# Kernel optimization log

Hardware: AMD Instinct MI355X
Metric: run time of the kernel (lower is better)

Reference implementation:

```python
import math
import jax, jax.numpy as jnp
import numpy as np

B, S, HID = 2, 2048, 1024
NH, HD = 16, 64            # num heads, head dim (HID = NH*HD)
NB, MAXD = 32, 128         # relative attention buckets / max distance
Q_SCALING = 1.0


def setup_inputs() -> dict:
    key = jax.random.key(0)
    ks = jax.random.split(key, 6)
    return {
        "hidden_states": jax.random.normal(ks[0], (B, S, HID), dtype=jnp.float32),
        "w_qkv": jax.random.normal(ks[1], (HID, 3 * HID), dtype=jnp.float32) * 0.02,
        "b_qkv": jax.random.normal(ks[2], (3 * HID,), dtype=jnp.float32) * 0.02,
        "w_dense": jax.random.normal(ks[3], (HID, HID), dtype=jnp.float32) * 0.02,
        "b_dense": jax.random.normal(ks[4], (HID,), dtype=jnp.float32) * 0.02,
        "rel_attn_table": jax.random.normal(ks[5], (NH, NB), dtype=jnp.float32) * 0.02,
    }


def _relative_position_bucket(q_len, k_len, num_buckets, max_distance):
    # Bidirectional T5-style buckets, matching compute_relative_bias.
    ctx = jnp.arange(q_len, dtype=jnp.int32)[:, None]
    mem = jnp.arange(k_len, dtype=jnp.int32)[None, :]
    rel = mem - ctx                                     # [Q, K]
    nb = num_buckets // 2
    buckets = jnp.where(rel > 0, nb, 0)
    rel = jnp.abs(rel)
    max_exact = nb // 2
    is_small = rel < max_exact
    # log path (clamp to >=1 to avoid log(0); masked by is_small anyway)
    tmp = jnp.log(jnp.maximum(rel, 1).astype(jnp.float32) / max_exact)
    large = tmp / math.log(max_distance / max_exact) * (nb - max_exact)
    large = max_exact + large.astype(jnp.int32)
    large = jnp.minimum(large, nb - 1)
    return buckets + jnp.where(is_small, rel, large)    # [Q, K]


def reference(hidden_states, w_qkv, b_qkv, w_dense, b_dense, rel_attn_table):
    b, s, _ = hidden_states.shape
    qkv = hidden_states @ w_qkv + b_qkv                 # [B, S, 3*HID]
    q, k, v = jnp.split(qkv, 3, axis=-1)
    q = q.reshape(b, s, NH, HD)
    k = k.reshape(b, s, NH, HD)
    v = v.reshape(b, s, NH, HD)

    norm = Q_SCALING * math.sqrt(HD)
    scores = jnp.einsum("bqhd,bkhd->bhqk", q, k) / norm  # [B, H, S, S]

    buckets = _relative_position_bucket(s, s, NB, MAXD)  # [Q, K] int32
    bias = rel_attn_table[:, buckets]                    # [H, Q, K]
    scores = scores + bias[None]

    probs = jax.nn.softmax(scores, axis=-1)
    ctx = jnp.einsum("bhqk,bkhd->bqhd", probs, v).reshape(b, s, HID)
    return ctx @ w_dense + b_dense
```

## Files before the change

### kernel.cpp

```cpp
#include <hip/hip_runtime.h>
#include <hip/hip_bf16.h>
#include <math.h>

#define S_ 2048

typedef __attribute__((ext_vector_type(8))) short bf16x8;
typedef __attribute__((ext_vector_type(4))) float f32x4;
typedef __attribute__((ext_vector_type(8))) unsigned short u16x8;
typedef __attribute__((ext_vector_type(4))) unsigned short u16x4;

__device__ inline unsigned short f2bf(float f) {
  union { float f; unsigned u; } x; x.f = f;
  unsigned r = x.u + 0x7fff + ((x.u >> 16) & 1);
  return (unsigned short)(r >> 16);
}

__device__ __forceinline__ void gll16(const unsigned short* g, unsigned short* l) {
  __builtin_amdgcn_global_load_lds(
      (const __attribute__((address_space(1))) unsigned int*)g,
      (__attribute__((address_space(3))) unsigned int*)l, 16, 0, 0);
}

__global__ void bias_table_kernel(const float* __restrict__ table,
                                  float* __restrict__ biasTab) {
  int idx = blockIdx.x * blockDim.x + threadIdx.x;
  if (idx >= 16 * 4096) return;
  int h = idx >> 12;
  int r = idx & 4095;
  int rel = r - 2047;
  int bucket = rel > 0 ? 16 : 0;
  int ar = rel < 0 ? -rel : rel;
  if (ar < 8) {
    bucket += ar;
  } else {
    float tmp = logf((float)ar / 8.0f);
    float lf = tmp / 2.7725887222397811f * 8.0f;
    int large = 8 + (int)lf;
    bucket += (large < 15 ? large : 15);
  }
  biasTab[idx] = table[h * 32 + bucket];
}

__global__ __launch_bounds__(256) void cvt_bf16_kernel(
    const float* __restrict__ in, unsigned short* __restrict__ out, int n8) {
  int i = blockIdx.x * blockDim.x + threadIdx.x;
  if (i >= n8) return;
  float4 a = ((const float4*)in)[i * 2];
  float4 b = ((const float4*)in)[i * 2 + 1];
  u16x8 o;
  o[0] = f2bf(a.x); o[1] = f2bf(a.y); o[2] = f2bf(a.z); o[3] = f2bf(a.w);
  o[4] = f2bf(b.x); o[5] = f2bf(b.y); o[6] = f2bf(b.z); o[7] = f2bf(b.w);
  *(u16x8*)&out[(size_t)i * 8] = o;
}

__global__ __launch_bounds__(256) void transpose_cvt_kernel(
    const float* __restrict__ in, unsigned short* __restrict__ out,
    int K, int N) {
  __shared__ unsigned short tile[64][72];
  const int k0 = blockIdx.y * 64, n0 = blockIdx.x * 64;
  const int tid = threadIdx.x;
  const int rr = tid >> 4, cc = (tid & 15) * 4;
#pragma unroll
  for (int p = 0; p < 4; ++p) {
    int k = rr + p * 16;
    float4 v = *(const float4*)&in[(size_t)(k0 + k) * N + n0 + cc];
    tile[k][cc + 0] = f2bf(v.x);
    tile[k][cc + 1] = f2bf(v.y);
    tile[k][cc + 2] = f2bf(v.z);
    tile[k][cc + 3] = f2bf(v.w);
  }
  __syncthreads();
#pragma unroll
  for (int p = 0; p < 4; ++p) {
    int n = rr + p * 16;
    u16x4 o;
    o[0] = tile[cc + 0][n];
    o[1] = tile[cc + 1][n];
    o[2] = tile[cc + 2][n];
    o[3] = tile[cc + 3][n];
    *(u16x4*)&out[(size_t)(n0 + n) * K + k0 + cc] = o;
  }
}

template <bool BF16OUT>
__global__ __launch_bounds__(256) void gemm_mfma_kernel(
    const unsigned short* __restrict__ A, const unsigned short* __restrict__ Bt,
    const float* __restrict__ bias, void* __restrict__ Cout,
    int M, int N, int K) {
  __shared__ __align__(16) unsigned short As[128 * 32];
  __shared__ __align__(16) unsigned short Bs[128 * 32];
  const int tid = threadIdx.x;
  const int wave = tid >> 6, lane = tid & 63;
  const int lg = lane >> 4, lr = lane & 15;
  const int m0 = blockIdx.y * 128, n0 = blockIdx.x * 128;
  const int wm = (wave & 1) * 64, wn = (wave >> 1) * 64;

  f32x4 acc[4][4] = {};

  const int r0 = tid >> 2;
  const int sw = ((tid & 3) ^ (r0 & 3)) << 3;
  const unsigned short* aP0 = A + (size_t)(m0 + r0) * K + sw;
  const unsigned short* aP1 = A + (size_t)(m0 + 64 + r0) * K + sw;
  const unsigned short* bP0 = Bt + (size_t)(n0 + r0) * K + sw;
  const unsigned short* bP1 = Bt + (size_t)(n0 + 64 + r0) * K + sw;
  unsigned short* ldsA0 = &As[(tid & ~63) * 8];
  unsigned short* ldsA1 = &As[(256 + (tid & ~63)) * 8];
  unsigned short* ldsB0 = &Bs[(tid & ~63) * 8];
  unsigned short* ldsB1 = &Bs[(256 + (tid & ~63)) * 8];

  const int swz = (lg ^ (lr & 3)) << 3;

  for (int kt = 0; kt < K; kt += 32) {
    __syncthreads();
    gll16(aP0 + kt, ldsA0);
    gll16(aP1 + kt, ldsA1);
    gll16(bP0 + kt, ldsB0);
    gll16(bP1 + kt, ldsB1);
    __syncthreads();
    bf16x8 af[4], bfr[4];
#pragma unroll
    for (int t = 0; t < 4; ++t) {
      af[t]  = *(const bf16x8*)&As[(wm + t * 16 + lr) * 32 + swz];
      bfr[t] = *(const bf16x8*)&Bs[(wn + t * 16 + lr) * 32 + swz];
    }
#pragma unroll
    for (int i = 0; i < 4; ++i)
#pragma unroll
      for (int j = 0; j < 4; ++j)
        acc[i][j] = __builtin_amdgcn_mfma_f32_16x16x32_bf16(
            af[i], bfr[j], acc[i][j], 0, 0, 0);
  }

  float bv[4];
#pragma unroll
  for (int j = 0; j < 4; ++j) bv[j] = bias[n0 + wn + j * 16 + lr];
#pragma unroll
  for (int i = 0; i < 4; ++i) {
#pragma unroll
    for (int j = 0; j < 4; ++j) {
#pragma unroll
      for (int r = 0; r < 4; ++r) {
        int row = m0 + wm + i * 16 + lg * 4 + r;
        int col = n0 + wn + j * 16 + lr;
        float val = acc[i][j][r] + bv[j];
        if constexpr (BF16OUT)
          ((unsigned short*)Cout)[(size_t)row * N + col] = f2bf(val);
        else
          ((float*)Cout)[(size_t)row * N + col] = val;
      }
    }
  }
}

__global__ __launch_bounds__(256) void vperm_kernel(
    const unsigned short* __restrict__ qkvb, unsigned short* __restrict__ vP) {
  const int t = blockIdx.x, h = blockIdx.y, bb = blockIdx.z;
  __shared__ unsigned short tile[64][72];
  const int tid = threadIdx.x;
  {
    int k = tid >> 2, c = (tid & 3) * 16;
    const unsigned short* src =
        qkvb + (size_t)(bb * S_ + t * 64 + k) * 3072 + 2048 + h * 64 + c;
    *(bf16x8*)&tile[k][c] = *(const bf16x8*)src;
    *(bf16x8*)&tile[k][c + 8] = *(const bf16x8*)(src + 8);
  }
  __syncthreads();
  const int d = tid >> 2, m0 = (tid & 3) * 16;
  unsigned short* dst =
      vP + ((size_t)((bb * 16 + h) * 64 + d)) * S_ + t * 64 + m0;
#pragma unroll
  for (int half = 0; half < 2; ++half) {
    u16x8 o;
#pragma unroll
    for (int j = 0; j < 8; ++j) {
      int m = m0 + half * 8 + j;
      int phys_s = m >> 3, e = m & 7;
      int s = phys_s ^ (d & 7);
      int w = s >> 2, lg = s & 3;
      int kw = w * 32 + (e >> 2) * 16 + lg * 4 + (e & 3);
      o[j] = tile[kw][d];
    }
    *(u16x8*)(dst + half * 8) = o;
  }
}

__global__ __launch_bounds__(512) void attn_mfma4_kernel(
    const unsigned short* __restrict__ qkvb, const unsigned short* __restrict__ vP,
    const float* __restrict__ biasTab, unsigned short* __restrict__ ctxb) {
  const int wg0 = blockIdx.x;
  const int wg = (wg0 & 7) * 64 + (wg0 >> 3);
  const int qt = wg & 15;
  const int h  = (wg >> 4) & 15;
  const int bb = wg >> 8;

  const int tid = threadIdx.x;
  const int wave = tid >> 6;
  const int lane = tid & 63;
  const int lg = lane >> 4;
  const int lr = lane & 15;

  __shared__ __align__(16) unsigned short Klds[2][4096];
  __shared__ __align__(16) unsigned short Vlds[2][4096];
  __shared__ float biasW[2][192];

  const int q0 = qt * 128;
  const int qw = q0 + wave * 16;

  bf16x8 qf[2];
#pragma unroll
  for (int kh = 0; kh < 2; ++kh)
    qf[kh] = *(const bf16x8*)(qkvb +
        (size_t)(bb * S_ + qw + lr) * 3072 + h * 64 + kh * 32 + lg * 8);

  float mrun = -1e30f;
  float lrun = 0.f;
  f32x4 ov[4] = {};

  const int kk = tid >> 3, kpb = tid & 7;
  const unsigned short* kptr = qkvb + (size_t)(bb * S_ + kk) * 3072 + 1024 +
                               h * 64 + (kpb ^ (kk & 7)) * 8;
  const unsigned short* vptr = vP + ((size_t)((bb * 16 + h) * 64 + (tid >> 3))) * S_ +
                               (tid & 7) * 8;
  const float* btabH = biasTab + h * 4096 + 2047;

  auto nonuni = [&](int tt) {
    int rl = tt * 64 - q0;
    return !((rl - 127 >= 91) || (rl + 63 <= -91));
  };

  gll16(kptr, &Klds[0][(tid & ~63) * 8]);
  gll16(vptr, &Vlds[0][(tid & ~63) * 8]);
  if (nonuni(0) && tid < 192) biasW[0][tid] = btabH[-q0 - 127 + tid];

  for (int t = 0; t < 32; ++t) {
    const int cur = t & 1;
    __syncthreads();

    if (t < 31) {
      const size_t kadv = (size_t)(t + 1) * 64 * 3072;
      gll16(kptr + kadv, &Klds[cur ^ 1][(tid & ~63) * 8]);
      gll16(vptr + (t + 1) * 64, &Vlds[cur ^ 1][(tid & ~63) * 8]);
      if (nonuni(t + 1) && tid < 192)
        biasW[cur ^ 1][tid] = btabH[(t + 1) * 64 - q0 - 127 + tid];
    }

    f32x4 sc[4] = {};
#pragma unroll
    for (int kt = 0; kt < 4; ++kt) {
      const unsigned short* kr = &Klds[cur][(kt * 16 + lr) * 64];
      bf16x8 kf0 = *(const bf16x8*)(kr + ((lg)     ^ (lr & 7)) * 8);
      bf16x8 kf1 = *(const bf16x8*)(kr + ((4 + lg) ^ (lr & 7)) * 8);
      sc[kt] = __builtin_amdgcn_mfma_f32_16x16x32_bf16(kf0, qf[0], sc[kt], 0, 0, 0);
      sc[kt] = __builtin_amdgcn_mfma_f32_16x16x32_bf16(kf1, qf[1], sc[kt], 0, 0, 0);
    }

    float pp[4][4];
    if (nonuni(t)) {
      const int bidx = 127 + lg * 4 - wave * 16 - lr;
#pragma unroll
      for (int kt = 0; kt < 4; ++kt)
#pragma unroll
        for (int r = 0; r < 4; ++r)
          pp[kt][r] = sc[kt][r] * 0.125f + biasW[cur][bidx + kt * 16 + r];
    } else {
      const float cb = btabH[t * 64 - q0];
#pragma unroll
      for (int kt = 0; kt < 4; ++kt)
#pragma unroll
        for (int r = 0; r < 4; ++r)
          pp[kt][r] = sc[kt][r] * 0.125f + cb;
    }

    float mx[8];
#pragma unroll
    for (int i = 0; i < 8; ++i)
      mx[i] = fmaxf(pp[i >> 1][(i & 1) * 2], pp[i >> 1][(i & 1) * 2 + 1]);
    float m01 = fmaxf(mx[0], mx[1]), m23 = fmaxf(mx[2], mx[3]);
    float m45 = fmaxf(mx[4], mx[5]), m67 = fmaxf(mx[6], mx[7]);
    float tm = fmaxf(fmaxf(m01, m23), fmaxf(m45, m67));
    tm = fmaxf(tm, __shfl_xor(tm, 16));
    tm = fmaxf(tm, __shfl_xor(tm, 32));

    if (!__all(tm <= mrun + 8.f)) {
      float mn = fmaxf(mrun, tm);
      float sfv = __expf(mrun - mn);
      mrun = mn;
      lrun *= sfv;
#pragma unroll
      for (int r = 0; r < 4; ++r) {
        float sq = __shfl(sfv, (lane & 48) | (lg * 4 + r));
#pragma unroll
        for (int db = 0; db < 4; ++db) ov[db][r] *= sq;
      }
    }

#pragma unroll
    for (int kt = 0; kt < 4; ++kt)
#pragma unroll
      for (int r = 0; r < 4; ++r)
        pp[kt][r] = __expf(pp[kt][r] - mrun);
    float s8[8];
#pragma unroll
    for (int i = 0; i < 8; ++i)
      s8[i] = pp[i >> 1][(i & 1) * 2] + pp[i >> 1][(i & 1) * 2 + 1];
    float s01 = s8[0] + s8[1], s23 = s8[2] + s8[3];
    float s45 = s8[4] + s8[5], s67 = s8[6] + s8[7];
    float rs = (s01 + s23) + (s45 + s67);
    rs += __shfl_xor(rs, 16);
    rs += __shfl_xor(rs, 32);
    lrun += rs;

    union { bf16x8 v; unsigned u[4]; } pk[2];
#pragma unroll
    for (int kh = 0; kh < 2; ++kh) {
      asm("v_cvt_pk_bf16_f32 %0, %1, %2"
          : "=v"(pk[kh].u[0]) : "v"(pp[2 * kh][0]), "v"(pp[2 * kh][1]));
      asm("v_cvt_pk_bf16_f32 %0, %1, %2"
          : "=v"(pk[kh].u[1]) : "v"(pp[2 * kh][2]), "v"(pp[2 * kh][3]));
      asm("v_cvt_pk_bf16_f32 %0, %1, %2"
          : "=v"(pk[kh].u[2]) : "v"(pp[2 * kh + 1][0]), "v"(pp[2 * kh + 1][1]));
      asm("v_cvt_pk_bf16_f32 %0, %1, %2"
          : "=v"(pk[kh].u[3]) : "v"(pp[2 * kh + 1][2]), "v"(pp[2 * kh + 1][3]));
    }

#pragma unroll
    for (int kh = 0; kh < 2; ++kh)
#pragma unroll
      for (int db = 0; db < 4; ++db) {
        bf16x8 vf = *(const bf16x8*)&Vlds[cur][
            (db * 16 + lr) * 64 + ((4 * kh + lg) ^ (lr & 7)) * 8];
        ov[db] = __builtin_amdgcn_mfma_f32_16x16x32_bf16(
            pk[kh].v, vf, ov[db], 0, 0, 0);
      }
  }

  float invl = 1.0f / lrun;
#pragma unroll
  for (int r = 0; r < 4; ++r) {
    float iv = __shfl(invl, (lane & 48) | (lg * 4 + r));
    size_t row = (size_t)(bb * S_ + qw + lg * 4 + r);
#pragma unroll
    for (int db = 0; db < 4; ++db)
      ctxb[row * 1024 + h * 64 + db * 16 + lr] = f2bf(ov[db][r] * iv);
  }
}

extern "C" void kernel_launch(void* const* d_in, const int* in_sizes, int n_in,
                              void* d_out, int out_size, void* d_ws, size_t ws_size,
                              hipStream_t stream) {
  const float* hs      = (const float*)d_in[0];
  const float* w_qkv   = (const float*)d_in[1];
  const float* b_qkv   = (const float*)d_in[2];
  const float* w_dense = (const float*)d_in[3];
  const float* b_dense = (const float*)d_in[4];
  const float* rtab    = (const float*)d_in[5];
  float* out = (float*)d_out;

  char* ws = (char*)d_ws;
  unsigned short* qkvb = (unsigned short*)ws;
  unsigned short* ctxb = (unsigned short*)(ws + (((size_t)24) << 20));
  unsigned short* hsb  = (unsigned short*)(ws + (((size_t)32) << 20));
  unsigned short* wqT  = (unsigned short*)(ws + (((size_t)40) << 20));
  unsigned short* wdT  = (unsigned short*)(ws + (((size_t)46) << 20));
  unsigned short* vP   = (unsigned short*)(ws + (((size_t)48) << 20));
  float* biasTab       = (float*)(ws + (((size_t)56) << 20));

  hipLaunchKernelGGL(bias_table_kernel, dim3(256), dim3(256), 0, stream,
                     rtab, biasTab);
  hipLaunchKernelGGL(cvt_bf16_kernel, dim3(2048), dim3(256), 0, stream,
                     hs, hsb, 4096 * 1024 / 8);
  hipLaunchKernelGGL(transpose_cvt_kernel, dim3(48, 16), dim3(256), 0, stream,
                     w_qkv, wqT, 1024, 3072);
  hipLaunchKernelGGL(transpose_cvt_kernel, dim3(16, 16), dim3(256), 0, stream,
                     w_dense, wdT, 1024, 1024);
  hipLaunchKernelGGL((gemm_mfma_kernel<true>), dim3(24, 32), dim3(256), 0, stream,
                     hsb, wqT, b_qkv, (void*)qkvb, 4096, 3072, 1024);
  hipLaunchKernelGGL(vperm_kernel, dim3(32, 16, 2), dim3(256), 0, stream,
                     qkvb, vP);
  hipLaunchKernelGGL(attn_mfma4_kernel, dim3(512), dim3(512), 0, stream,
                     qkvb, vP, biasTab, ctxb);
  hipLaunchKernelGGL((gemm_mfma_kernel<false>), dim3(8, 32), dim3(256), 0, stream,
                     ctxb, wdT, b_dense, (void*)out, 4096, 1024, 1024);
}
```

Before: 154.1 us.

## Switch attention to 32x32x16 MFMA with 4 waves of 32 query rows

Rewrites the flash-attention kernel to use 32x32x16 bf16 MFMA instructions. Each of 4 waves now owns 32 query rows, where before 8 waves each held 16. The V permutation kernel's layout and the K/V LDS loads change to match the new fragment layout, and row reductions now need only one cross-lane shuffle. The intent is to cut shuffle, softmax-rescale and LDS-read overhead per MFMA, at the cost of fewer waves per block, higher register pressure, and a scalar f2bf conversion replacing the packed cvt instruction.

```diff
diff --git a/kernel.cpp b/kernel.cpp
--- a/kernel.cpp
+++ b/kernel.cpp
@@ -6,6 +6,7 @@
 
 typedef __attribute__((ext_vector_type(8))) short bf16x8;
 typedef __attribute__((ext_vector_type(4))) float f32x4;
+typedef __attribute__((ext_vector_type(16))) float f32x16;
 typedef __attribute__((ext_vector_type(8))) unsigned short u16x8;
 typedef __attribute__((ext_vector_type(4))) unsigned short u16x4;
 
@@ -174,17 +175,17 @@
 #pragma unroll
     for (int j = 0; j < 8; ++j) {
       int m = m0 + half * 8 + j;
-      int phys_s = m >> 3, e = m & 7;
-      int s = phys_s ^ (d & 7);
-      int w = s >> 2, lg = s & 3;
-      int kw = w * 32 + (e >> 2) * 16 + lg * 4 + (e & 3);
+      int ps = m >> 3, e = m & 7;
+      int ls = ps ^ (d & 7);
+      int c = ls >> 1, hi2 = ls & 1;
+      int kw = 16 * c + (e & 3) + 8 * (e >> 2) + 4 * hi2;
       o[j] = tile[kw][d];
     }
     *(u16x8*)(dst + half * 8) = o;
   }
 }
 
-__global__ __launch_bounds__(512) void attn_mfma4_kernel(
+__global__ __launch_bounds__(256) void attn_mfma5_kernel(
     const unsigned short* __restrict__ qkvb, const unsigned short* __restrict__ vP,
     const float* __restrict__ biasTab, unsigned short* __restrict__ ctxb) {
   const int wg0 = blockIdx.x;
@@ -196,31 +197,34 @@
   const int tid = threadIdx.x;
   const int wave = tid >> 6;
   const int lane = tid & 63;
-  const int lg = lane >> 4;
-  const int lr = lane & 15;
+  const int l5 = lane & 31;
+  const int hi = lane >> 5;
 
   __shared__ __align__(16) unsigned short Klds[2][4096];
   __shared__ __align__(16) unsigned short Vlds[2][4096];
   __shared__ float biasW[2][192];
 
   const int q0 = qt * 128;
-  const int qw = q0 + wave * 16;
-
-  bf16x8 qf[2];
-#pragma unroll
-  for (int kh = 0; kh < 2; ++kh)
-    qf[kh] = *(const bf16x8*)(qkvb +
-        (size_t)(bb * S_ + qw + lr) * 3072 + h * 64 + kh * 32 + lg * 8);
+  const int qg = q0 + wave * 32 + l5;
+
+  bf16x8 qf[4];
+#pragma unroll
+  for (int c = 0; c < 4; ++c)
+    qf[c] = *(const bf16x8*)(qkvb +
+        (size_t)(bb * S_ + qg) * 3072 + h * 64 + c * 16 + hi * 8);
 
   float mrun = -1e30f;
   float lrun = 0.f;
-  f32x4 ov[4] = {};
-
-  const int kk = tid >> 3, kpb = tid & 7;
-  const unsigned short* kptr = qkvb + (size_t)(bb * S_ + kk) * 3072 + 1024 +
-                               h * 64 + (kpb ^ (kk & 7)) * 8;
-  const unsigned short* vptr = vP + ((size_t)((bb * 16 + h) * 64 + (tid >> 3))) * S_ +
-                               (tid & 7) * 8;
+  f32x16 ov0 = {}, ov1 = {};
+
+  const int kk = tid >> 3, kps = tid & 7;
+  const unsigned short* kptr0 = qkvb + (size_t)(bb * S_ + kk) * 3072 + 1024 +
+                                h * 64 + ((kps ^ (kk & 7)) * 8);
+  const unsigned short* kptr1 = qkvb + (size_t)(bb * S_ + 32 + kk) * 3072 + 1024 +
+                                h * 64 + ((kps ^ (kk & 7)) * 8);
+  const unsigned short* vPbase = vP + ((size_t)((bb * 16 + h) * 64)) * S_;
+  const unsigned short* vptr0 = vPbase + (size_t)kk * S_ + kps * 8;
+  const unsigned short* vptr1 = vPbase + (size_t)(32 + kk) * S_ + kps * 8;
   const float* btabH = biasTab + h * 4096 + 2047;
 
   auto nonuni = [&](int tt) {
@@ -228,8 +232,10 @@
     return !((rl - 127 >= 91) || (rl + 63 <= -91));
   };
 
-  gll16(kptr, &Klds[0][(tid & ~63) * 8]);
-  gll16(vptr, &Vlds[0][(tid & ~63) * 8]);
+  gll16(kptr0, &Klds[0][(tid & ~63) * 8]);
+  gll16(kptr1, &Klds[0][2048 + (tid & ~63) * 8]);
+  gll16(vptr0, &Vlds[0][(tid & ~63) * 8]);
+  gll16(vptr1, &Vlds[0][2048 + (tid & ~63) * 8]);
   if (nonuni(0) && tid < 192) biasW[0][tid] = btabH[-q0 - 127 + tid];
 
   for (int t = 0; t < 32; ++t) {
@@ -238,47 +244,50 @@
 
     if (t < 31) {
       const size_t kadv = (size_t)(t + 1) * 64 * 3072;
-      gll16(kptr + kadv, &Klds[cur ^ 1][(tid & ~63) * 8]);
-      gll16(vptr + (t + 1) * 64, &Vlds[cur ^ 1][(tid & ~63) * 8]);
+      gll16(kptr0 + kadv, &Klds[cur ^ 1][(tid & ~63) * 8]);
+      gll16(kptr1 + kadv, &Klds[cur ^ 1][2048 + (tid & ~63) * 8]);
+      gll16(vptr0 + (t + 1) * 64, &Vlds[cur ^ 1][(tid & ~63) * 8]);
+      gll16(vptr1 + (t + 1) * 64, &Vlds[cur ^ 1][2048 + (tid & ~63) * 8]);
       if (nonuni(t + 1) && tid < 192)
         biasW[cur ^ 1][tid] = btabH[(t + 1) * 64 - q0 - 127 + tid];
     }
 
-    f32x4 sc[4] = {};
-#pragma unroll
-    for (int kt = 0; kt < 4; ++kt) {
-      const unsigned short* kr = &Klds[cur][(kt * 16 + lr) * 64];
-      bf16x8 kf0 = *(const bf16x8*)(kr + ((lg)     ^ (lr & 7)) * 8);
-      bf16x8 kf1 = *(const bf16x8*)(kr + ((4 + lg) ^ (lr & 7)) * 8);
-      sc[kt] = __builtin_amdgcn_mfma_f32_16x16x32_bf16(kf0, qf[0], sc[kt], 0, 0, 0);
-      sc[kt] = __builtin_amdgcn_mfma_f32_16x16x32_bf16(kf1, qf[1], sc[kt], 0, 0, 0);
-    }
-
-    float pp[4][4];
+    f32x16 sc0 = {}, sc1 = {};
+#pragma unroll
+    for (int c = 0; c < 4; ++c) {
+      const int slot = ((2 * c + hi) ^ (l5 & 7)) * 8;
+      bf16x8 kf0 = *(const bf16x8*)&Klds[cur][l5 * 64 + slot];
+      bf16x8 kf1 = *(const bf16x8*)&Klds[cur][(32 + l5) * 64 + slot];
+      sc0 = __builtin_amdgcn_mfma_f32_32x32x16_bf16(kf0, qf[c], sc0, 0, 0, 0);
+      sc1 = __builtin_amdgcn_mfma_f32_32x32x16_bf16(kf1, qf[c], sc1, 0, 0, 0);
+    }
+
+    float p0[16], p1[16];
     if (nonuni(t)) {
-      const int bidx = 127 + lg * 4 - wave * 16 - lr;
-#pragma unroll
-      for (int kt = 0; kt < 4; ++kt)
-#pragma unroll
-        for (int r = 0; r < 4; ++r)
-          pp[kt][r] = sc[kt][r] * 0.125f + biasW[cur][bidx + kt * 16 + r];
+      const int jb = 127 - wave * 32 - l5 + 4 * hi;
+#pragma unroll
+      for (int r = 0; r < 16; ++r) {
+        const int off = (r & 3) + 8 * (r >> 2);
+        p0[r] = sc0[r] * 0.125f + biasW[cur][jb + off];
+        p1[r] = sc1[r] * 0.125f + biasW[cur][jb + 32 + off];
+      }
     } else {
       const float cb = btabH[t * 64 - q0];
 #pragma unroll
-      for (int kt = 0; kt < 4; ++kt)
-#pragma unroll
-        for (int r = 0; r < 4; ++r)
-          pp[kt][r] = sc[kt][r] * 0.125f + cb;
-    }
-
-    float mx[8];
-#pragma unroll
-    for (int i = 0; i < 8; ++i)
-      mx[i] = fmaxf(pp[i >> 1][(i & 1) * 2], pp[i >> 1][(i & 1) * 2 + 1]);
-    float m01 = fmaxf(mx[0], mx[1]), m23 = fmaxf(mx[2], mx[3]);
-    float m45 = fmaxf(mx[4], mx[5]), m67 = fmaxf(mx[6], mx[7]);
-    float tm = fmaxf(fmaxf(m01, m23), fmaxf(m45, m67));
-    tm = fmaxf(tm, __shfl_xor(tm, 16));
+      for (int r = 0; r < 16; ++r) {
+        p0[r] = sc0[r] * 0.125f + cb;
+        p1[r] = sc1[r] * 0.125f + cb;
+      }
+    }
+
+    float mx[16];
+#pragma unroll
+    for (int r = 0; r < 16; ++r) mx[r] = fmaxf(p0[r], p1[r]);
+#pragma unroll
+    for (int s = 8; s > 0; s >>= 1)
+#pragma unroll
+      for (int r = 0; r < s; ++r) mx[r] = fmaxf(mx[r], mx[r + s]);
+    float tm = mx[0];
     tm = fmaxf(tm, __shfl_xor(tm, 32));
 
     if (!__all(tm <= mrun + 8.f)) {
@@ -287,61 +296,58 @@
       mrun = mn;
       lrun *= sfv;
 #pragma unroll
-      for (int r = 0; r < 4; ++r) {
-        float sq = __shfl(sfv, (lane & 48) | (lg * 4 + r));
-#pragma unroll
-        for (int db = 0; db < 4; ++db) ov[db][r] *= sq;
-      }
-    }
-
-#pragma unroll
-    for (int kt = 0; kt < 4; ++kt)
-#pragma unroll
-      for (int r = 0; r < 4; ++r)
-        pp[kt][r] = __expf(pp[kt][r] - mrun);
-    float s8[8];
-#pragma unroll
-    for (int i = 0; i < 8; ++i)
-      s8[i] = pp[i >> 1][(i & 1) * 2] + pp[i >> 1][(i & 1) * 2 + 1];
-    float s01 = s8[0] + s8[1], s23 = s8[2] + s8[3];
-    float s45 = s8[4] + s8[5], s67 = s8[6] + s8[7];
-    float rs = (s01 + s23) + (s45 + s67);
-    rs += __shfl_xor(rs, 16);
+      for (int r = 0; r < 16; ++r) { ov0[r] *= sfv; ov1[r] *= sfv; }
+    }
+
+#pragma unroll
+    for (int r = 0; r < 16; ++r) {
+      p0[r] = __expf(p0[r] - mrun);
+      p1[r] = __expf(p1[r] - mrun);
+    }
+    float sm[16];
+#pragma unroll
+    for (int r = 0; r < 16; ++r) sm[r] = p0[r] + p1[r];
+#pragma unroll
+    for (int s = 8; s > 0; s >>= 1)
+#pragma unroll
+      for (int r = 0; r < s; ++r) sm[r] += sm[r + s];
+    float rs = sm[0];
     rs += __shfl_xor(rs, 32);
     lrun += rs;
 
-    union { bf16x8 v; unsigned u[4]; } pk[2];
-#pragma unroll
-    for (int kh = 0; kh < 2; ++kh) {
-      asm("v_cvt_pk_bf16_f32 %0, %1, %2"
-          : "=v"(pk[kh].u[0]) : "v"(pp[2 * kh][0]), "v"(pp[2 * kh][1]));
-      asm("v_cvt_pk_bf16_f32 %0, %1, %2"
-          : "=v"(pk[kh].u[1]) : "v"(pp[2 * kh][2]), "v"(pp[2 * kh][3]));
-      asm("v_cvt_pk_bf16_f32 %0, %1, %2"
-          : "=v"(pk[kh].u[2]) : "v"(pp[2 * kh + 1][0]), "v"(pp[2 * kh + 1][1]));
-      asm("v_cvt_pk_bf16_f32 %0, %1, %2"
-          : "=v"(pk[kh].u[3]) : "v"(pp[2 * kh + 1][2]), "v"(pp[2 * kh + 1][3]));
-    }
-
-#pragma unroll
-    for (int kh = 0; kh < 2; ++kh)
-#pragma unroll
-      for (int db = 0; db < 4; ++db) {
-        bf16x8 vf = *(const bf16x8*)&Vlds[cur][
-            (db * 16 + lr) * 64 + ((4 * kh + lg) ^ (lr & 7)) * 8];
-        ov[db] = __builtin_amdgcn_mfma_f32_16x16x32_bf16(
-            pk[kh].v, vf, ov[db], 0, 0, 0);
+    bf16x8 pk[4];
+#pragma unroll
+    for (int c = 0; c < 4; ++c) {
+      const int rb = 8 * (c & 1);
+#pragma unroll
+      for (int e = 0; e < 8; ++e) {
+        float pv = (c < 2) ? p0[rb + e] : p1[rb + e];
+        pk[c][e] = (short)f2bf(pv);
       }
-  }
-
-  float invl = 1.0f / lrun;
-#pragma unroll
-  for (int r = 0; r < 4; ++r) {
-    float iv = __shfl(invl, (lane & 48) | (lg * 4 + r));
-    size_t row = (size_t)(bb * S_ + qw + lg * 4 + r);
-#pragma unroll
-    for (int db = 0; db < 4; ++db)
-      ctxb[row * 1024 + h * 64 + db * 16 + lr] = f2bf(ov[db][r] * iv);
+    }
+
+#pragma unroll
+    for (int c = 0; c < 4; ++c) {
+      const int slot = ((2 * c + hi) ^ (l5 & 7)) * 8;
+      bf16x8 vt0 = *(const bf16x8*)&Vlds[cur][l5 * 64 + slot];
+      bf16x8 vt1 = *(const bf16x8*)&Vlds[cur][(32 + l5) * 64 + slot];
+      ov0 = __builtin_amdgcn_mfma_f32_32x32x16_bf16(vt0, pk[c], ov0, 0, 0, 0);
+      ov1 = __builtin_amdgcn_mfma_f32_32x32x16_bf16(vt1, pk[c], ov1, 0, 0, 0);
+    }
+  }
+
+  const float invl = 1.0f / lrun;
+  const size_t rowb = (size_t)(bb * S_ + qg) * 1024 + h * 64;
+#pragma unroll
+  for (int g = 0; g < 4; ++g) {
+    u16x4 a, b;
+#pragma unroll
+    for (int j = 0; j < 4; ++j) {
+      a[j] = f2bf(ov0[4 * g + j] * invl);
+      b[j] = f2bf(ov1[4 * g + j] * invl);
+    }
+    *(u16x4*)&ctxb[rowb + 8 * g + 4 * hi] = a;
+    *(u16x4*)&ctxb[rowb + 32 + 8 * g + 4 * hi] = b;
   }
 }
 
@@ -377,7 +383,7 @@
                      hsb, wqT, b_qkv, (void*)qkvb, 4096, 3072, 1024);
   hipLaunchKernelGGL(vperm_kernel, dim3(32, 16, 2), dim3(256), 0, stream,
                      qkvb, vP);
-  hipLaunchKernelGGL(attn_mfma4_kernel, dim3(512), dim3(512), 0, stream,
+  hipLaunchKernelGGL(attn_mfma5_kernel, dim3(512), dim3(256), 0, stream,
                      qkvb, vP, biasTab, ctxb);
   hipLaunchKernelGGL((gemm_mfma_kernel<false>), dim3(8, 32), dim3(256), 0, stream,
                      ctxb, wdT, b_dense, (void*)out, 4096, 1024, 1024);
```

Measured after the change: 164.7 us. 1.07x slower.
